# Kernel tuning notes

Measured on AMD Instinct MI355X. Metric: run time of the kernel, lower is better.

The kernel has to match this reference:

```python
import jax, jax.numpy as jnp
import numpy as np
from jax import lax

T, B, F, H = 128, 256, 512, 1024
NEG_SLOPE = 0.01  # torch LeakyReLU default


def leaky_relu(x):
    return jnp.where(x >= 0, x, NEG_SLOPE * x)


def setup_inputs() -> dict:
    key = jax.random.key(0)
    ks = jax.random.split(key, 10)
    s1 = 1.0 / np.sqrt(F)
    sh = 1.0 / np.sqrt(H)
    return {
        "x": jax.random.normal(ks[0], (T, B, F), dtype=jnp.float32),
        "dones": jax.random.randint(ks[1], (T, B), 0, 2, dtype=jnp.int32),
        "W1": jax.random.uniform(ks[2], (H, F), jnp.float32, -s1, s1),
        "b1": jax.random.uniform(ks[3], (H,), jnp.float32, -s1, s1),
        "W_ih": jax.random.uniform(ks[4], (4 * H, H), jnp.float32, -sh, sh),
        "W_hh": jax.random.uniform(ks[5], (4 * H, H), jnp.float32, -sh, sh),
        "b_ih": jax.random.uniform(ks[6], (4 * H,), jnp.float32, -sh, sh),
        "b_hh": jax.random.uniform(ks[7], (4 * H,), jnp.float32, -sh, sh),
        "Wv": jax.random.uniform(ks[8], (1, H), jnp.float32, -sh, sh),
        "bv": jax.random.uniform(ks[9], (1,), jnp.float32, -sh, sh),
    }


def _forward(x, dones, W1, b1, W_ih, W_hh, b_ih, b_hh, Wv, bv):
    # shared_net: Linear + LeakyReLU, applied to all timesteps at once
    shared = leaky_relu(jnp.einsum("tbf,hf->tbh", x, W1) + b1)  # [T,B,H]
    # precompute input contribution to all gates (i,f,g,o order as in torch)
    x_gates = jnp.einsum("tbh,gh->tbg", shared, W_ih) + b_ih + b_hh  # [T,B,4H]
    reset = (dones == 0).astype(x.dtype)[:, :, None]  # [T,B,1], 0 where done

    def step(carry, inp):
        h, c = carry  # [B,H] each
        xg, m = inp
        # mask-reset hidden state where episode ended, then detach (torch .detach())
        h = lax.stop_gradient(h * m)
        c = lax.stop_gradient(c * m)
        gates = xg + h @ W_hh.T  # [B,4H]
        i, f, g, o = jnp.split(gates, 4, axis=-1)
        i = jax.nn.sigmoid(i)
        f = jax.nn.sigmoid(f)
        g = jnp.tanh(g)
        o = jax.nn.sigmoid(o)
        c = f * c + i * g
        h = o * jnp.tanh(c)
        return (h, c), h

    h0 = jnp.zeros((x.shape[1], W_hh.shape[1]), x.dtype)
    (hT, cT), hs = lax.scan(step, (h0, h0), (x_gates, reset))
    value = leaky_relu(hs) @ Wv.T + bv  # [T,B,1]
    hidden = jnp.stack([hT, cT], axis=0)  # [2*num_layers, B, H]
    return value, hidden


def reference(x, dones, W1, b1, W_ih, W_hh, b_ih, b_hh, Wv, bv):
    return _forward(x, dones, W1, b1, W_ih, W_hh, b_ih, b_hh, Wv, bv)
```

## Files before the change

### kernel.cpp

```cpp
#include <hip/hip_runtime.h>
#include <cstdint>
#include <cstddef>

#define T_DIM 128
#define B_DIM 256
#define F_DIM 512
#define H_DIM 1024
#define G_DIM 4096

typedef unsigned short u16;
typedef unsigned short u16x8 __attribute__((ext_vector_type(8)));
typedef unsigned short u16x4 __attribute__((ext_vector_type(4)));
typedef __bf16 bf16x8 __attribute__((ext_vector_type(8)));
typedef float f32x4 __attribute__((ext_vector_type(4)));

__device__ __forceinline__ float bf2f(u16 u) {
    union { unsigned v; float f; } x; x.v = ((unsigned)u) << 16; return x.f;
}
__device__ __forceinline__ u16 f2bf(float f) {
    union { float f; unsigned v; } x; x.f = f;
    return (u16)((x.v + 0x7fffu + ((x.v >> 16) & 1u)) >> 16);
}

__device__ __forceinline__ f32x4 mfma16(u16x8 a, u16x8 b, f32x4 c) {
    return __builtin_amdgcn_mfma_f32_16x16x32_bf16(
        __builtin_bit_cast(bf16x8, a), __builtin_bit_cast(bf16x8, b), c, 0, 0, 0);
}

template <int AUX>
__device__ __forceinline__ void gl_lds16(const void* g, void* s) {
    __builtin_amdgcn_global_load_lds(
        (const __attribute__((address_space(1))) void*)g,
        (__attribute__((address_space(3))) void*)s, 16, 0, AUX);
}

__device__ __forceinline__ float sigm(float x) { return 1.0f / (1.0f + __expf(-x)); }
__device__ __forceinline__ float tanh_fast(float x) {
    float e = __expf(2.0f * x);
    return 1.0f - 2.0f / (e + 1.0f);
}

template <int EPI>
__global__ __launch_bounds__(256) void gemm_bt128(
    const u16* __restrict__ A, const u16* __restrict__ B,
    const float* __restrict__ bias, u16* __restrict__ C, int K, int N) {
    __shared__ __align__(16) u16 smem[128 * 136];
    u16* lA = smem;
    u16* lB = smem + 8192;
    const int lane = threadIdx.x & 63;
    const int wave = threadIdx.x >> 6;
    const int wr = wave >> 1, wc = wave & 1;
    const int bm = blockIdx.x, bn = blockIdx.y;
    f32x4 acc[4][4] = {};
    const int srow = lane >> 3;
    const int scol = (lane & 7) * 8;
    const u16* Abase = A + (size_t)(bm * 128 + srow) * K + scol;
    const u16* Bbase = B + (size_t)(bn * 128 + srow) * K + scol;

    for (int k0 = 0; k0 < K; k0 += 64) {
#pragma unroll
        for (int j = 0; j < 4; ++j) {
            int chunk = wave * 4 + j;
            gl_lds16<0>(Abase + (size_t)(chunk * 8) * K + k0, lA + chunk * 512);
            gl_lds16<0>(Bbase + (size_t)(chunk * 8) * K + k0, lB + chunk * 512);
        }
        __syncthreads();
        const u16* pA = lA + (wr * 64 + (lane & 15)) * 64 + (lane >> 4) * 8;
        const u16* pB = lB + (wc * 64 + (lane & 15)) * 64 + (lane >> 4) * 8;
#pragma unroll
        for (int kk = 0; kk < 2; ++kk) {
            u16x8 a[4], b[4];
#pragma unroll
            for (int m = 0; m < 4; ++m) a[m] = *(const u16x8*)(pA + m * 1024 + kk * 32);
#pragma unroll
            for (int n = 0; n < 4; ++n) b[n] = *(const u16x8*)(pB + n * 1024 + kk * 32);
#pragma unroll
            for (int m = 0; m < 4; ++m)
#pragma unroll
                for (int n = 0; n < 4; ++n)
                    acc[m][n] = mfma16(a[m], b[n], acc[m][n]);
        }
        __syncthreads();
    }
#pragma unroll
    for (int n = 0; n < 4; ++n) {
        int cc = wc * 64 + n * 16 + (lane & 15);
        float bv = bias[bn * 128 + cc];
#pragma unroll
        for (int m = 0; m < 4; ++m) {
            int rr = wr * 64 + m * 16 + ((lane >> 4) * 4);
#pragma unroll
            for (int i = 0; i < 4; ++i) {
                float v = acc[m][n][i] + bv;
                if (EPI == 1) v = (v >= 0.0f) ? v : 0.01f * v;
                smem[(rr + i) * 136 + cc] = f2bf(v);
            }
        }
    }
    __syncthreads();
#pragma unroll
    for (int p = 0; p < 8; ++p) {
        int rr = p * 16 + wave * 4 + (lane >> 4);
        int cc = (lane & 15) * 8;
        u16x8 v = *(const u16x8*)(smem + rr * 136 + cc);
        *(u16x8*)(C + (size_t)(bm * 128 + rr) * N + bn * 128 + cc) = v;
    }
}


template <int AUX>
__device__ __forceinline__ void stage_chunk(const char* panel, char* buf, int kc,
                                            int wave, int lane) {
#pragma unroll
    for (int j = 0; j < 8; ++j) {
        int hr = wave * 8 + j;
        int r = hr * 2 + (lane >> 5);
        int sc = ((lane & 31) * 16) ^ ((r & 7) << 4);
        gl_lds16<AUX>(panel + (size_t)r * 2048 + kc * 512 + sc, buf + (size_t)hr * 1024);
    }
}

__global__ __launch_bounds__(256, 1) void lstm_seq(
    const u16* __restrict__ xg, const u16* __restrict__ Whh,
    const int* __restrict__ dones, const float* __restrict__ Wv,
    u16* __restrict__ h0, u16* __restrict__ h1,
    float* __restrict__ cbuf, float* __restrict__ hbuf,
    float* __restrict__ value, int* __restrict__ flags,
    float* __restrict__ vpartial, int t0, int nt, int first) {
    __shared__ __align__(16) char sm[65536];
    float* lepi = (float*)sm;
    const int tid = threadIdx.x;
    const int lane = tid & 63, wave = tid >> 6;
    const int bm = blockIdx.x & 3, bn = blockIdx.x >> 2;
    const int sw = (lane & 7) << 4;

    u16x8 breg[32];
    {
        const char* wp = (const char*)(Whh + (size_t)(bn * 64) * H_DIM);
        const int rlb = wave * 16 + (lane & 15);
#pragma unroll
        for (int kc = 0; kc < 4; ++kc) {
            char* buf = sm + (kc & 1) * 32768;
            stage_chunk<0>(wp, buf, kc, wave, lane);
            __syncthreads();
#pragma unroll
            for (int s2 = 0; s2 < 8; ++s2) {
                int kb2 = s2 * 64 + (lane >> 4) * 16;
                breg[kc * 8 + s2] = *(const u16x8*)(buf + rlb * 512 + (kb2 ^ sw));
            }
            __syncthreads();
        }
    }

    const int r = tid & 63;
    const int ublk = tid >> 6;
    const int bg = bm * 64 + r;
    const int ucol = bn * 16 + ublk * 4;
    float wv[4], c[4];
#pragma unroll
    for (int uu = 0; uu < 4; ++uu) wv[uu] = Wv[ucol + uu];
    if (first) {
        c[0] = c[1] = c[2] = c[3] = 0.0f;
    } else {
        float4 cv = *(const float4*)(cbuf + (size_t)bg * H_DIM + ucol);
        c[0] = cv.x; c[1] = cv.y; c[2] = cv.z; c[3] = cv.w;
    }

    for (int tt = 0; tt < nt; ++tt) {
        const int t = t0 + tt;
        const u16* hin = (t & 1) ? h1 : h0;
        u16* hout = (t & 1) ? h0 : h1;
        const char* hp = (const char*)(hin + (size_t)(bm * 64) * H_DIM);

        const int done = dones[t * B_DIM + bg];
        u16x4 xv[4];
#pragma unroll
        for (int uu = 0; uu < 4; ++uu)
            xv[uu] = *(const u16x4*)(xg + (size_t)tt * B_DIM * G_DIM +
                                     (size_t)bg * G_DIM + bn * 64 + (ublk * 4 + uu) * 4);

        if (t > 0 && tid < 64) {
            while (__hip_atomic_load(&flags[bm * 64 + tid], __ATOMIC_RELAXED,
                                     __HIP_MEMORY_SCOPE_AGENT) < t)
                __builtin_amdgcn_s_sleep(1);
        }
        __syncthreads();

        stage_chunk<17>(hp, sm, 0, wave, lane);
        if (t > 0 && tid < 64) {
            const float* vp = vpartial + (size_t)((t - 1) & 1) * 65536 +
                              (size_t)(bm * 64 + bn) * 256 + lane * 4;
            union { unsigned long long u; float f[2]; } ua, ub;
            ua.u = __hip_atomic_load((const unsigned long long*)vp, __ATOMIC_RELAXED,
                                     __HIP_MEMORY_SCOPE_AGENT);
            ub.u = __hip_atomic_load((const unsigned long long*)(vp + 2), __ATOMIC_RELAXED,
                                     __HIP_MEMORY_SCOPE_AGENT);
            float s = ua.f[0] + ua.f[1] + ub.f[0] + ub.f[1];
#pragma unroll
            for (int m2 = 32; m2 >= 1; m2 >>= 1) s += __shfl_xor(s, m2);
            if (tid == 0) value[(t - 1) * B_DIM + bm * 64 + bn] += s;
        }
        __syncthreads();

        f32x4 acc[4] = {};
#pragma unroll
        for (int kc = 0; kc < 4; ++kc) {
            char* buf = sm + (kc & 1) * 32768;
            if (kc < 3) stage_chunk<17>(hp, sm + ((kc + 1) & 1) * 32768, kc + 1, wave, lane);
#pragma unroll
            for (int s2 = 0; s2 < 8; ++s2) {
                int kb2 = s2 * 64 + (lane >> 4) * 16;
#pragma unroll
                for (int m = 0; m < 4; ++m) {
                    u16x8 a = *(const u16x8*)(buf + (m * 16 + (lane & 15)) * 512 + (kb2 ^ sw));
                    acc[m] = mfma16(a, breg[kc * 8 + s2], acc[m]);
                }
            }
            __syncthreads();
        }

#pragma unroll
        for (int m = 0; m < 4; ++m)
#pragma unroll
            for (int i = 0; i < 4; ++i)
                lepi[(m * 16 + (lane >> 4) * 4 + i) * 65 + wave * 16 + (lane & 15)] = acc[m][i];
        __syncthreads();

        const float mb = (done == 0) ? 1.0f : 0.0f;
        float vpart = 0.0f;
        u16x4 hb;
        float hf[4];
#pragma unroll
        for (int uu = 0; uu < 4; ++uu) {
            const float* gp = &lepi[r * 65 + (ublk * 4 + uu) * 4];
            float gi = bf2f(xv[uu][0]) + mb * gp[0];
            float gf = bf2f(xv[uu][1]) + mb * gp[1];
            float gg = bf2f(xv[uu][2]) + mb * gp[2];
            float go = bf2f(xv[uu][3]) + mb * gp[3];
            float i_ = sigm(gi), f_ = sigm(gf), g_ = tanh_fast(gg), o_ = sigm(go);
            float cn = f_ * (mb * c[uu]) + i_ * g_;
            float hn = o_ * tanh_fast(cn);
            c[uu] = cn; hf[uu] = hn;
            hb[uu] = f2bf(hn);
            float lr = (hn >= 0.0f) ? hn : 0.01f * hn;
            vpart += lr * wv[uu];
        }
        __hip_atomic_store((unsigned long long*)(hout + (size_t)bg * H_DIM + ucol),
                           __builtin_bit_cast(unsigned long long, hb),
                           __ATOMIC_RELAXED, __HIP_MEMORY_SCOPE_AGENT);
        if (t == T_DIM - 1)
            *(float4*)(hbuf + (size_t)bg * H_DIM + ucol) = make_float4(hf[0], hf[1], hf[2], hf[3]);
        __hip_atomic_store(&vpartial[(size_t)(t & 1) * 65536 + (size_t)bg * 256 + bn * 4 + ublk],
                           vpart, __ATOMIC_RELAXED, __HIP_MEMORY_SCOPE_AGENT);

        __syncthreads();
        if (tid == 0)
            __hip_atomic_store(&flags[bm * 64 + bn], t + 1, __ATOMIC_RELAXED,
                               __HIP_MEMORY_SCOPE_AGENT);
    }
    *(float4*)(cbuf + (size_t)bg * H_DIM + ucol) = make_float4(c[0], c[1], c[2], c[3]);

    if (t0 + nt == T_DIM && tid < 64) {
        while (__hip_atomic_load(&flags[bm * 64 + tid], __ATOMIC_RELAXED,
                                 __HIP_MEMORY_SCOPE_AGENT) < T_DIM)
            __builtin_amdgcn_s_sleep(1);
        const float* vp = vpartial + (size_t)((T_DIM - 1) & 1) * 65536 +
                          (size_t)(bm * 64 + bn) * 256 + lane * 4;
        union { unsigned long long u; float f[2]; } ua, ub;
        ua.u = __hip_atomic_load((const unsigned long long*)vp, __ATOMIC_RELAXED,
                                 __HIP_MEMORY_SCOPE_AGENT);
        ub.u = __hip_atomic_load((const unsigned long long*)(vp + 2), __ATOMIC_RELAXED,
                                 __HIP_MEMORY_SCOPE_AGENT);
        float s = ua.f[0] + ua.f[1] + ub.f[0] + ub.f[1];
#pragma unroll
        for (int m2 = 32; m2 >= 1; m2 >>= 1) s += __shfl_xor(s, m2);
        if (tid == 0) value[(T_DIM - 1) * B_DIM + bm * 64 + bn] += s;
    }
}

__global__ void k_cast_bf16(const float* __restrict__ in, u16* __restrict__ out, int n4) {
    int i = blockIdx.x * 256 + threadIdx.x;
    if (i < n4) {
        float4 v = *(const float4*)(in + (size_t)i * 4);
        u16x4 o;
        o[0] = f2bf(v.x); o[1] = f2bf(v.y); o[2] = f2bf(v.z); o[3] = f2bf(v.w);
        *(u16x4*)(out + (size_t)i * 4) = o;
    }
}

__global__ void k_permute_w(const float* __restrict__ W, u16* __restrict__ Wp) {
    int row = blockIdx.x;
    int rin = (row & 3) * H_DIM + (row >> 2);
    int c = threadIdx.x * 4;
    float4 v = *(const float4*)(W + (size_t)rin * H_DIM + c);
    u16x4 o;
    o[0] = f2bf(v.x); o[1] = f2bf(v.y); o[2] = f2bf(v.z); o[3] = f2bf(v.w);
    *(u16x4*)(Wp + (size_t)row * H_DIM + c) = o;
}

__global__ void k_prep_bias(const float* __restrict__ b_ih, const float* __restrict__ b_hh,
                            float* __restrict__ bc) {
    int i = blockIdx.x * 256 + threadIdx.x;
    int n = i >> 2, q = i & 3;
    bc[i] = b_ih[q * H_DIM + n] + b_hh[q * H_DIM + n];
}

__global__ void k_init(float* __restrict__ value, const float* __restrict__ bv,
                       u16* __restrict__ h0, int* __restrict__ flags) {
    int i = blockIdx.x * 256 + threadIdx.x;
    if (i < B_DIM * H_DIM) h0[i] = 0;
    if (i < T_DIM * B_DIM) value[i] = *bv;
    if (i < 256) flags[i] = 0;
}

extern "C" void kernel_launch(void* const* d_in, const int* in_sizes, int n_in,
                              void* d_out, int out_size, void* d_ws, size_t ws_size,
                              hipStream_t stream) {
    const float* x     = (const float*)d_in[0];
    const int*   dones = (const int*)d_in[1];
    const float* W1    = (const float*)d_in[2];
    const float* b1    = (const float*)d_in[3];
    const float* W_ih  = (const float*)d_in[4];
    const float* W_hh  = (const float*)d_in[5];
    const float* b_ih  = (const float*)d_in[6];
    const float* b_hh  = (const float*)d_in[7];
    const float* Wv    = (const float*)d_in[8];
    const float* bv    = (const float*)d_in[9];

    float* out   = (float*)d_out;
    float* value = out;
    float* hbuf  = out + (size_t)T_DIM * B_DIM;
    float* cbuf  = hbuf + (size_t)B_DIM * H_DIM;

    const size_t per_nt = (size_t)(F_DIM + H_DIM + G_DIM) * B_DIM * 2;
    const size_t fixed = (size_t)H_DIM * F_DIM * 2 + 2 * (size_t)G_DIM * H_DIM * 2 +
                         G_DIM * 4 + 2 * (size_t)B_DIM * H_DIM * 2 +
                         2 * 65536 * 4 + 8192;
    int nt = 2;
    for (int cand = 16; cand >= 2; cand >>= 1)
        if (fixed + (size_t)cand * per_nt + 65536 <= ws_size) { nt = cand; break; }

    char* ws = (char*)d_ws;
    size_t off = 0;
    auto alloc = [&](size_t bytes) {
        void* p = ws + off;
        off = (off + bytes + 255) & ~(size_t)255;
        return p;
    };
    u16*   x_bf   = (u16*)alloc((size_t)nt * B_DIM * F_DIM * 2);
    u16*   shr    = (u16*)alloc((size_t)nt * B_DIM * H_DIM * 2);
    u16*   xg     = (u16*)alloc((size_t)nt * B_DIM * G_DIM * 2);
    u16*   W1b    = (u16*)alloc((size_t)H_DIM * F_DIM * 2);
    u16*   Wihp   = (u16*)alloc((size_t)G_DIM * H_DIM * 2);
    u16*   Whhp   = (u16*)alloc((size_t)G_DIM * H_DIM * 2);
    float* bcomb  = (float*)alloc((size_t)G_DIM * 4);
    u16*   hping  = (u16*)alloc((size_t)B_DIM * H_DIM * 2);
    u16*   hpong  = (u16*)alloc((size_t)B_DIM * H_DIM * 2);
    int*   flags  = (int*)alloc(256 * 4);
    float* vpart  = (float*)alloc(2 * 65536 * 4);

    k_cast_bf16<<<(H_DIM * F_DIM / 4) / 256, 256, 0, stream>>>(W1, W1b, H_DIM * F_DIM / 4);
    k_permute_w<<<G_DIM, 256, 0, stream>>>(W_ih, Wihp);
    k_permute_w<<<G_DIM, 256, 0, stream>>>(W_hh, Whhp);
    k_prep_bias<<<G_DIM / 256, 256, 0, stream>>>(b_ih, b_hh, bcomb);
    k_init<<<(B_DIM * H_DIM) / 256, 256, 0, stream>>>(value, bv, hping, flags);

    for (int t0 = 0; t0 < T_DIM; t0 += nt) {
        int m = nt * B_DIM;
        int n4 = m * F_DIM / 4;
        k_cast_bf16<<<n4 / 256, 256, 0, stream>>>(x + (size_t)t0 * B_DIM * F_DIM, x_bf, n4);
        gemm_bt128<1><<<dim3(m / 128, H_DIM / 128), 256, 0, stream>>>(
            x_bf, W1b, b1, shr, F_DIM, H_DIM);
        gemm_bt128<0><<<dim3(m / 128, G_DIM / 128), 256, 0, stream>>>(
            shr, Wihp, bcomb, xg, H_DIM, G_DIM);

        lstm_seq<<<256, 256, 0, stream>>>(
            xg, Whhp, dones, Wv, hping, hpong, cbuf, hbuf, value, flags, vpart,
            t0, nt, (t0 == 0) ? 1 : 0);
    }
}
```

Before: 1.727 ms.

## Widen LSTM recurrence blocks to 512 threads and enlarge timestep chunks

The persistent recurrent kernel now runs 128 blocks of 512 threads. Each block owns 128 gate columns (32 hidden units) and holds twice the W_hh slice in registers, loaded straight from global memory instead of through LDS. Each timestep now spins on 32 peer flags instead of 64, and the value reduction is spread across two waves. The host also allows up to 64 timesteps per chunk, so fewer GEMM and kernel launches are issued. The cost is fewer CUs used in the latency-bound recurrence and more per-block work, and the final barrier sequence is now executed by only some waves, which may be fragile.

```diff
diff --git a/kernel.cpp b/kernel.cpp
--- a/kernel.cpp
+++ b/kernel.cpp
@@ -109,18 +109,20 @@
 
 
 template <int AUX>
-__device__ __forceinline__ void stage_chunk(const char* panel, char* buf, int kc,
-                                            int wave, int lane) {
-#pragma unroll
-    for (int j = 0; j < 8; ++j) {
-        int hr = wave * 8 + j;
+__device__ __forceinline__ void stage_chunk8(const char* panel, char* buf, int kc,
+                                             int wave, int lane) {
+#pragma unroll
+    for (int j = 0; j < 4; ++j) {
+        int hr = wave * 4 + j;
         int r = hr * 2 + (lane >> 5);
         int sc = ((lane & 31) * 16) ^ ((r & 7) << 4);
         gl_lds16<AUX>(panel + (size_t)r * 2048 + kc * 512 + sc, buf + (size_t)hr * 1024);
     }
 }
 
-__global__ __launch_bounds__(256, 1) void lstm_seq(
+#define LEPI_STRIDE 132
+
+__global__ __launch_bounds__(512, 1) void lstm_seq(
     const u16* __restrict__ xg, const u16* __restrict__ Whh,
     const int* __restrict__ dones, const float* __restrict__ Wv,
     u16* __restrict__ h0, u16* __restrict__ h1,
@@ -136,26 +138,17 @@
 
     u16x8 breg[32];
     {
-        const char* wp = (const char*)(Whh + (size_t)(bn * 64) * H_DIM);
-        const int rlb = wave * 16 + (lane & 15);
-#pragma unroll
-        for (int kc = 0; kc < 4; ++kc) {
-            char* buf = sm + (kc & 1) * 32768;
-            stage_chunk<0>(wp, buf, kc, wave, lane);
-            __syncthreads();
-#pragma unroll
-            for (int s2 = 0; s2 < 8; ++s2) {
-                int kb2 = s2 * 64 + (lane >> 4) * 16;
-                breg[kc * 8 + s2] = *(const u16x8*)(buf + rlb * 512 + (kb2 ^ sw));
-            }
-            __syncthreads();
-        }
+        const u16* wrow = Whh + (size_t)(bn * 128 + wave * 16 + (lane & 15)) * H_DIM +
+                          (lane >> 4) * 8;
+#pragma unroll
+        for (int s = 0; s < 32; ++s)
+            breg[s] = *(const u16x8*)(wrow + s * 32);
     }
 
     const int r = tid & 63;
     const int ublk = tid >> 6;
     const int bg = bm * 64 + r;
-    const int ucol = bn * 16 + ublk * 4;
+    const int ucol = bn * 32 + ublk * 4;
     float wv[4], c[4];
 #pragma unroll
     for (int uu = 0; uu < 4; ++uu) wv[uu] = Wv[ucol + uu];
@@ -177,19 +170,20 @@
 #pragma unroll
         for (int uu = 0; uu < 4; ++uu)
             xv[uu] = *(const u16x4*)(xg + (size_t)tt * B_DIM * G_DIM +
-                                     (size_t)bg * G_DIM + bn * 64 + (ublk * 4 + uu) * 4);
-
-        if (t > 0 && tid < 64) {
-            while (__hip_atomic_load(&flags[bm * 64 + tid], __ATOMIC_RELAXED,
+                                     (size_t)bg * G_DIM + bn * 128 + (ublk * 4 + uu) * 4);
+
+        if (t > 0 && tid < 32) {
+            while (__hip_atomic_load(&flags[bm * 32 + tid], __ATOMIC_RELAXED,
                                      __HIP_MEMORY_SCOPE_AGENT) < t)
                 __builtin_amdgcn_s_sleep(1);
         }
         __syncthreads();
 
-        stage_chunk<17>(hp, sm, 0, wave, lane);
-        if (t > 0 && tid < 64) {
+        stage_chunk8<17>(hp, sm, 0, wave, lane);
+        if (t > 0 && tid < 128) {
+            const int grow = bm * 64 + bn * 2 + (tid >> 6);
             const float* vp = vpartial + (size_t)((t - 1) & 1) * 65536 +
-                              (size_t)(bm * 64 + bn) * 256 + lane * 4;
+                              (size_t)grow * 256 + (tid & 63) * 4;
             union { unsigned long long u; float f[2]; } ua, ub;
             ua.u = __hip_atomic_load((const unsigned long long*)vp, __ATOMIC_RELAXED,
                                      __HIP_MEMORY_SCOPE_AGENT);
@@ -198,7 +192,7 @@
             float s = ua.f[0] + ua.f[1] + ub.f[0] + ub.f[1];
 #pragma unroll
             for (int m2 = 32; m2 >= 1; m2 >>= 1) s += __shfl_xor(s, m2);
-            if (tid == 0) value[(t - 1) * B_DIM + bm * 64 + bn] += s;
+            if ((tid & 63) == 0) value[(t - 1) * B_DIM + grow] += s;
         }
         __syncthreads();
 
@@ -206,7 +200,7 @@
 #pragma unroll
         for (int kc = 0; kc < 4; ++kc) {
             char* buf = sm + (kc & 1) * 32768;
-            if (kc < 3) stage_chunk<17>(hp, sm + ((kc + 1) & 1) * 32768, kc + 1, wave, lane);
+            if (kc < 3) stage_chunk8<17>(hp, sm + ((kc + 1) & 1) * 32768, kc + 1, wave, lane);
 #pragma unroll
             for (int s2 = 0; s2 < 8; ++s2) {
                 int kb2 = s2 * 64 + (lane >> 4) * 16;
@@ -223,7 +217,8 @@
         for (int m = 0; m < 4; ++m)
 #pragma unroll
             for (int i = 0; i < 4; ++i)
-                lepi[(m * 16 + (lane >> 4) * 4 + i) * 65 + wave * 16 + (lane & 15)] = acc[m][i];
+                lepi[(m * 16 + (lane >> 4) * 4 + i) * LEPI_STRIDE + wave * 16 + (lane & 15)] =
+                    acc[m][i];
         __syncthreads();
 
         const float mb = (done == 0) ? 1.0f : 0.0f;
@@ -232,7 +227,7 @@
         float hf[4];
 #pragma unroll
         for (int uu = 0; uu < 4; ++uu) {
-            const float* gp = &lepi[r * 65 + (ublk * 4 + uu) * 4];
+            const float* gp = &lepi[r * LEPI_STRIDE + (ublk * 4 + uu) * 4];
             float gi = bf2f(xv[uu][0]) + mb * gp[0];
             float gf = bf2f(xv[uu][1]) + mb * gp[1];
             float gg = bf2f(xv[uu][2]) + mb * gp[2];
@@ -250,31 +245,40 @@
                            __ATOMIC_RELAXED, __HIP_MEMORY_SCOPE_AGENT);
         if (t == T_DIM - 1)
             *(float4*)(hbuf + (size_t)bg * H_DIM + ucol) = make_float4(hf[0], hf[1], hf[2], hf[3]);
-        __hip_atomic_store(&vpartial[(size_t)(t & 1) * 65536 + (size_t)bg * 256 + bn * 4 + ublk],
+        __hip_atomic_store(&vpartial[(size_t)(t & 1) * 65536 + (size_t)bg * 256 + bn * 8 + ublk],
                            vpart, __ATOMIC_RELAXED, __HIP_MEMORY_SCOPE_AGENT);
 
         __syncthreads();
         if (tid == 0)
-            __hip_atomic_store(&flags[bm * 64 + bn], t + 1, __ATOMIC_RELAXED,
+            __hip_atomic_store(&flags[bm * 32 + bn], t + 1, __ATOMIC_RELAXED,
                                __HIP_MEMORY_SCOPE_AGENT);
     }
     *(float4*)(cbuf + (size_t)bg * H_DIM + ucol) = make_float4(c[0], c[1], c[2], c[3]);
 
-    if (t0 + nt == T_DIM && tid < 64) {
-        while (__hip_atomic_load(&flags[bm * 64 + tid], __ATOMIC_RELAXED,
-                                 __HIP_MEMORY_SCOPE_AGENT) < T_DIM)
-            __builtin_amdgcn_s_sleep(1);
-        const float* vp = vpartial + (size_t)((T_DIM - 1) & 1) * 65536 +
-                          (size_t)(bm * 64 + bn) * 256 + lane * 4;
-        union { unsigned long long u; float f[2]; } ua, ub;
-        ua.u = __hip_atomic_load((const unsigned long long*)vp, __ATOMIC_RELAXED,
-                                 __HIP_MEMORY_SCOPE_AGENT);
-        ub.u = __hip_atomic_load((const unsigned long long*)(vp + 2), __ATOMIC_RELAXED,
-                                 __HIP_MEMORY_SCOPE_AGENT);
-        float s = ua.f[0] + ua.f[1] + ub.f[0] + ub.f[1];
-#pragma unroll
-        for (int m2 = 32; m2 >= 1; m2 >>= 1) s += __shfl_xor(s, m2);
-        if (tid == 0) value[(T_DIM - 1) * B_DIM + bm * 64 + bn] += s;
+    if (t0 + nt == T_DIM && tid < 128) {
+        if (tid < 32) {
+            while (__hip_atomic_load(&flags[bm * 32 + tid], __ATOMIC_RELAXED,
+                                     __HIP_MEMORY_SCOPE_AGENT) < T_DIM)
+                __builtin_amdgcn_s_sleep(1);
+        }
+        __builtin_amdgcn_s_barrier();
+    }
+    if (t0 + nt == T_DIM) {
+        __syncthreads();
+        if (tid < 128) {
+            const int grow = bm * 64 + bn * 2 + (tid >> 6);
+            const float* vp = vpartial + (size_t)((T_DIM - 1) & 1) * 65536 +
+                              (size_t)grow * 256 + (tid & 63) * 4;
+            union { unsigned long long u; float f[2]; } ua, ub;
+            ua.u = __hip_atomic_load((const unsigned long long*)vp, __ATOMIC_RELAXED,
+                                     __HIP_MEMORY_SCOPE_AGENT);
+            ub.u = __hip_atomic_load((const unsigned long long*)(vp + 2), __ATOMIC_RELAXED,
+                                     __HIP_MEMORY_SCOPE_AGENT);
+            float s = ua.f[0] + ua.f[1] + ub.f[0] + ub.f[1];
+#pragma unroll
+            for (int m2 = 32; m2 >= 1; m2 >>= 1) s += __shfl_xor(s, m2);
+            if ((tid & 63) == 0) value[(T_DIM - 1) * B_DIM + grow] += s;
+        }
     }
 }
 
@@ -337,8 +341,9 @@
                          G_DIM * 4 + 2 * (size_t)B_DIM * H_DIM * 2 +
                          2 * 65536 * 4 + 8192;
     int nt = 2;
-    for (int cand = 16; cand >= 2; cand >>= 1)
+    for (int cand = 64; cand >= 2; cand >>= 1)
         if (fixed + (size_t)cand * per_nt + 65536 <= ws_size) { nt = cand; break; }
+    if (nt > T_DIM) nt = T_DIM;
 
     char* ws = (char*)d_ws;
     size_t off = 0;
@@ -374,7 +379,7 @@
         gemm_bt128<0><<<dim3(m / 128, G_DIM / 128), 256, 0, stream>>>(
             shr, Wihp, bcomb, xg, H_DIM, G_DIM);
 
-        lstm_seq<<<256, 256, 0, stream>>>(
+        lstm_seq<<<128, 512, 0, stream>>>(
             xg, Whhp, dones, Wv, hping, hpong, cbuf, hbuf, value, flags, vpart,
             t0, nt, (t0 == 0) ? 1 : 0);
     }
```

New measurement: 1.747 ms. Within noise of the previous version (+1.2%).

## Retile hidden-state layout, stage full h panel in 128KB LDS, coalesce stores

Applied to the files above, without the earlier changes.

Changes the global layout of the ping-pong hidden-state buffer and the value partials to a tiled form. Each block now writes its h tile and value partials with contiguous, coalesced atomic stores after staging them through LDS. When 128KB of dynamic shared memory is available, the whole 64x1024 h panel is loaded in one pass with a single barrier instead of four double-buffered chunks. W_hh fragments are also loaded straight into registers, and the time-chunk size can grow to 64, which cuts the number of launches. The extra LDS round-trip and barrier in the epilogue add some latency to every step.

```diff
diff --git a/kernel.cpp b/kernel.cpp
--- a/kernel.cpp
+++ b/kernel.cpp
@@ -13,6 +13,7 @@
 typedef unsigned short u16x4 __attribute__((ext_vector_type(4)));
 typedef __bf16 bf16x8 __attribute__((ext_vector_type(8)));
 typedef float f32x4 __attribute__((ext_vector_type(4)));
+typedef unsigned long long u64;
 
 __device__ __forceinline__ float bf2f(u16 u) {
     union { unsigned v; float f; } x; x.v = ((unsigned)u) << 16; return x.f;
@@ -107,19 +108,7 @@
     }
 }
 
-
-template <int AUX>
-__device__ __forceinline__ void stage_chunk(const char* panel, char* buf, int kc,
-                                            int wave, int lane) {
-#pragma unroll
-    for (int j = 0; j < 8; ++j) {
-        int hr = wave * 8 + j;
-        int r = hr * 2 + (lane >> 5);
-        int sc = ((lane & 31) * 16) ^ ((r & 7) << 4);
-        gl_lds16<AUX>(panel + (size_t)r * 2048 + kc * 512 + sc, buf + (size_t)hr * 1024);
-    }
-}
-
+template <int FULL>
 __global__ __launch_bounds__(256, 1) void lstm_seq(
     const u16* __restrict__ xg, const u16* __restrict__ Whh,
     const int* __restrict__ dones, const float* __restrict__ Wv,
@@ -127,29 +116,20 @@
     float* __restrict__ cbuf, float* __restrict__ hbuf,
     float* __restrict__ value, int* __restrict__ flags,
     float* __restrict__ vpartial, int t0, int nt, int first) {
-    __shared__ __align__(16) char sm[65536];
+    extern __shared__ __align__(16) char sm[];
     float* lepi = (float*)sm;
+    char* hbB = sm + 20480;
+    float* vpB = (float*)(sm + 24576);
     const int tid = threadIdx.x;
     const int lane = tid & 63, wave = tid >> 6;
     const int bm = blockIdx.x & 3, bn = blockIdx.x >> 2;
-    const int sw = (lane & 7) << 4;
 
     u16x8 breg[32];
     {
-        const char* wp = (const char*)(Whh + (size_t)(bn * 64) * H_DIM);
-        const int rlb = wave * 16 + (lane & 15);
-#pragma unroll
-        for (int kc = 0; kc < 4; ++kc) {
-            char* buf = sm + (kc & 1) * 32768;
-            stage_chunk<0>(wp, buf, kc, wave, lane);
-            __syncthreads();
-#pragma unroll
-            for (int s2 = 0; s2 < 8; ++s2) {
-                int kb2 = s2 * 64 + (lane >> 4) * 16;
-                breg[kc * 8 + s2] = *(const u16x8*)(buf + rlb * 512 + (kb2 ^ sw));
-            }
-            __syncthreads();
-        }
+        const u16* wrow = Whh + (size_t)(bn * 64 + wave * 16 + (lane & 15)) * H_DIM +
+                          (lane >> 4) * 8;
+#pragma unroll
+        for (int s = 0; s < 32; ++s) breg[s] = *(const u16x8*)(wrow + s * 32);
     }
 
     const int r = tid & 63;
@@ -166,11 +146,13 @@
         c[0] = cv.x; c[1] = cv.y; c[2] = cv.z; c[3] = cv.w;
     }
 
+    const int rl = lane & 15;
+    const int ko = (lane >> 4) * 16;
+
     for (int tt = 0; tt < nt; ++tt) {
         const int t = t0 + tt;
-        const u16* hin = (t & 1) ? h1 : h0;
-        u16* hout = (t & 1) ? h0 : h1;
-        const char* hp = (const char*)(hin + (size_t)(bm * 64) * H_DIM);
+        const char* hinB = (const char*)((t & 1) ? h1 : h0);
+        u16* houtB = (t & 1) ? h0 : h1;
 
         const int done = dones[t * B_DIM + bg];
         u16x4 xv[4];
@@ -186,38 +168,85 @@
         }
         __syncthreads();
 
-        stage_chunk<17>(hp, sm, 0, wave, lane);
-        if (t > 0 && tid < 64) {
-            const float* vp = vpartial + (size_t)((t - 1) & 1) * 65536 +
-                              (size_t)(bm * 64 + bn) * 256 + lane * 4;
-            union { unsigned long long u; float f[2]; } ua, ub;
-            ua.u = __hip_atomic_load((const unsigned long long*)vp, __ATOMIC_RELAXED,
-                                     __HIP_MEMORY_SCOPE_AGENT);
-            ub.u = __hip_atomic_load((const unsigned long long*)(vp + 2), __ATOMIC_RELAXED,
-                                     __HIP_MEMORY_SCOPE_AGENT);
-            float s = ua.f[0] + ua.f[1] + ub.f[0] + ub.f[1];
-#pragma unroll
-            for (int m2 = 32; m2 >= 1; m2 >>= 1) s += __shfl_xor(s, m2);
-            if (tid == 0) value[(t - 1) * B_DIM + bm * 64 + bn] += s;
-        }
-        __syncthreads();
-
         f32x4 acc[4] = {};
-#pragma unroll
-        for (int kc = 0; kc < 4; ++kc) {
-            char* buf = sm + (kc & 1) * 32768;
-            if (kc < 3) stage_chunk<17>(hp, sm + ((kc + 1) & 1) * 32768, kc + 1, wave, lane);
-#pragma unroll
-            for (int s2 = 0; s2 < 8; ++s2) {
-                int kb2 = s2 * 64 + (lane >> 4) * 16;
+        if (FULL) {
+#pragma unroll
+            for (int l = 0; l < 32; ++l) {
+                int o = l * 4096 + wave * 1024 + lane * 16;
+                int row = o >> 11;
+                int cg = (o & 2047) ^ ((row & 7) << 4);
+                gl_lds16<17>(hinB + (size_t)(cg >> 5) * 8192 + bm * 2048 + row * 32 + (cg & 31),
+                             sm + o);
+            }
+            if (t > 0 && tid < 64) {
+                const float* vp = vpartial + (size_t)((t - 1) & 1) * 65536 +
+                                  (size_t)lane * 1024 + (size_t)(bm * 64 + bn) * 4;
+                union { u64 u; float f[2]; } ua, ub;
+                ua.u = __hip_atomic_load((const u64*)vp, __ATOMIC_RELAXED,
+                                         __HIP_MEMORY_SCOPE_AGENT);
+                ub.u = __hip_atomic_load((const u64*)(vp + 2), __ATOMIC_RELAXED,
+                                         __HIP_MEMORY_SCOPE_AGENT);
+                float s = ua.f[0] + ua.f[1] + ub.f[0] + ub.f[1];
+#pragma unroll
+                for (int m2 = 32; m2 >= 1; m2 >>= 1) s += __shfl_xor(s, m2);
+                if (tid == 0) value[(t - 1) * B_DIM + bm * 64 + bn] += s;
+            }
+            __syncthreads();
+
+#pragma unroll
+            for (int s = 0; s < 32; ++s) {
 #pragma unroll
                 for (int m = 0; m < 4; ++m) {
-                    u16x8 a = *(const u16x8*)(buf + (m * 16 + (lane & 15)) * 512 + (kb2 ^ sw));
-                    acc[m] = mfma16(a, breg[kc * 8 + s2], acc[m]);
+                    int row = m * 16 + rl;
+                    u16x8 a = *(const u16x8*)(sm + row * 2048 +
+                                              ((s * 64 + ko) ^ ((row & 7) << 4)));
+                    acc[m] = mfma16(a, breg[s], acc[m]);
                 }
             }
+        } else {
+            auto stage = [&](int kc, char* buf) {
+#pragma unroll
+                for (int l = 0; l < 8; ++l) {
+                    int o = l * 4096 + wave * 1024 + lane * 16;
+                    int row = o >> 9;
+                    int cg = (kc << 9) + ((o & 511) ^ ((row & 7) << 4));
+                    gl_lds16<17>(hinB + (size_t)(cg >> 5) * 8192 + bm * 2048 + row * 32 +
+                                 (cg & 31), buf + o);
+                }
+            };
+            stage(0, sm);
+            if (t > 0 && tid < 64) {
+                const float* vp = vpartial + (size_t)((t - 1) & 1) * 65536 +
+                                  (size_t)lane * 1024 + (size_t)(bm * 64 + bn) * 4;
+                union { u64 u; float f[2]; } ua, ub;
+                ua.u = __hip_atomic_load((const u64*)vp, __ATOMIC_RELAXED,
+                                         __HIP_MEMORY_SCOPE_AGENT);
+                ub.u = __hip_atomic_load((const u64*)(vp + 2), __ATOMIC_RELAXED,
+                                         __HIP_MEMORY_SCOPE_AGENT);
+                float s = ua.f[0] + ua.f[1] + ub.f[0] + ub.f[1];
+#pragma unroll
+                for (int m2 = 32; m2 >= 1; m2 >>= 1) s += __shfl_xor(s, m2);
+                if (tid == 0) value[(t - 1) * B_DIM + bm * 64 + bn] += s;
+            }
             __syncthreads();
-        }
+#pragma unroll
+            for (int kc = 0; kc < 4; ++kc) {
+                char* buf = sm + (kc & 1) * 32768;
+                if (kc < 3) stage(kc + 1, sm + ((kc + 1) & 1) * 32768);
+#pragma unroll
+                for (int s2 = 0; s2 < 8; ++s2) {
+#pragma unroll
+                    for (int m = 0; m < 4; ++m) {
+                        int row = m * 16 + rl;
+                        u16x8 a = *(const u16x8*)(buf + row * 512 +
+                                                  ((s2 * 64 + ko) ^ ((row & 7) << 4)));
+                        acc[m] = mfma16(a, breg[kc * 8 + s2], acc[m]);
+                    }
+                }
+                __syncthreads();
+            }
+        }
+        __syncthreads();
 
 #pragma unroll
         for (int m = 0; m < 4; ++m)
@@ -245,14 +274,25 @@
             float lr = (hn >= 0.0f) ? hn : 0.01f * hn;
             vpart += lr * wv[uu];
         }
-        __hip_atomic_store((unsigned long long*)(hout + (size_t)bg * H_DIM + ucol),
-                           __builtin_bit_cast(unsigned long long, hb),
-                           __ATOMIC_RELAXED, __HIP_MEMORY_SCOPE_AGENT);
+        *(u16x4*)(hbB + r * 32 + ublk * 8) = hb;
+        vpB[r * 4 + ublk] = vpart;
         if (t == T_DIM - 1)
             *(float4*)(hbuf + (size_t)bg * H_DIM + ucol) = make_float4(hf[0], hf[1], hf[2], hf[3]);
-        __hip_atomic_store(&vpartial[(size_t)(t & 1) * 65536 + (size_t)bg * 256 + bn * 4 + ublk],
-                           vpart, __ATOMIC_RELAXED, __HIP_MEMORY_SCOPE_AGENT);
-
+        __syncthreads();
+
+        {
+            u64 hv = *(const u64*)(hbB + tid * 8);
+            __hip_atomic_store((u64*)((char*)houtB + (size_t)bn * 8192 + bm * 2048 + tid * 8),
+                               hv, __ATOMIC_RELAXED, __HIP_MEMORY_SCOPE_AGENT);
+            if (tid < 64) {
+                const u64* pv = (const u64*)vpB + tid * 2;
+                u64 v0 = pv[0], v1 = pv[1];
+                float* dv = vpartial + (size_t)(t & 1) * 65536 + (size_t)bn * 1024 +
+                            bm * 256 + tid * 4;
+                __hip_atomic_store((u64*)dv, v0, __ATOMIC_RELAXED, __HIP_MEMORY_SCOPE_AGENT);
+                __hip_atomic_store((u64*)dv + 1, v1, __ATOMIC_RELAXED, __HIP_MEMORY_SCOPE_AGENT);
+            }
+        }
         __syncthreads();
         if (tid == 0)
             __hip_atomic_store(&flags[bm * 64 + bn], t + 1, __ATOMIC_RELAXED,
@@ -265,11 +305,10 @@
                                  __HIP_MEMORY_SCOPE_AGENT) < T_DIM)
             __builtin_amdgcn_s_sleep(1);
         const float* vp = vpartial + (size_t)((T_DIM - 1) & 1) * 65536 +
-                          (size_t)(bm * 64 + bn) * 256 + lane * 4;
-        union { unsigned long long u; float f[2]; } ua, ub;
-        ua.u = __hip_atomic_load((const unsigned long long*)vp, __ATOMIC_RELAXED,
-                                 __HIP_MEMORY_SCOPE_AGENT);
-        ub.u = __hip_atomic_load((const unsigned long long*)(vp + 2), __ATOMIC_RELAXED,
+                          (size_t)lane * 1024 + (size_t)(bm * 64 + bn) * 4;
+        union { u64 u; float f[2]; } ua, ub;
+        ua.u = __hip_atomic_load((const u64*)vp, __ATOMIC_RELAXED, __HIP_MEMORY_SCOPE_AGENT);
+        ub.u = __hip_atomic_load((const u64*)(vp + 2), __ATOMIC_RELAXED,
                                  __HIP_MEMORY_SCOPE_AGENT);
         float s = ua.f[0] + ua.f[1] + ub.f[0] + ub.f[1];
 #pragma unroll
@@ -337,8 +376,9 @@
                          G_DIM * 4 + 2 * (size_t)B_DIM * H_DIM * 2 +
                          2 * 65536 * 4 + 8192;
     int nt = 2;
-    for (int cand = 16; cand >= 2; cand >>= 1)
+    for (int cand = 64; cand >= 2; cand >>= 1)
         if (fixed + (size_t)cand * per_nt + 65536 <= ws_size) { nt = cand; break; }
+    if (nt > T_DIM) nt = T_DIM;
 
     char* ws = (char*)d_ws;
     size_t off = 0;
@@ -359,6 +399,10 @@
     int*   flags  = (int*)alloc(256 * 4);
     float* vpart  = (float*)alloc(2 * 65536 * 4);
 
+    int full = (hipFuncSetAttribute(reinterpret_cast<const void*>(&lstm_seq<1>),
+                                    hipFuncAttributeMaxDynamicSharedMemorySize,
+                                    131072) == hipSuccess) ? 1 : 0;
+
     k_cast_bf16<<<(H_DIM * F_DIM / 4) / 256, 256, 0, stream>>>(W1, W1b, H_DIM * F_DIM / 4);
     k_permute_w<<<G_DIM, 256, 0, stream>>>(W_ih, Wihp);
     k_permute_w<<<G_DIM, 256, 0, stream>>>(W_hh, Whhp);
@@ -374,8 +418,13 @@
         gemm_bt128<0><<<dim3(m / 128, G_DIM / 128), 256, 0, stream>>>(
             shr, Wihp, bcomb, xg, H_DIM, G_DIM);
 
-        lstm_seq<<<256, 256, 0, stream>>>(
-            xg, Whhp, dones, Wv, hping, hpong, cbuf, hbuf, value, flags, vpart,
-            t0, nt, (t0 == 0) ? 1 : 0);
-    }
-}
+        if (full)
+            lstm_seq<1><<<256, 256, 131072, stream>>>(
+                xg, Whhp, dones, Wv, hping, hpong, cbuf, hbuf, value, flags, vpart,
+                t0, nt, (t0 == 0) ? 1 : 0);
+        else
+            lstm_seq<0><<<256, 256, 65536, stream>>>(
+                xg, Whhp, dones, Wv, hping, hpong, cbuf, hbuf, value, flags, vpart,
+                t0, nt, (t0 == 0) ? 1 : 0);
+    }
+}
```

Result: slower. 1.982 ms (+14.8%).

## Block-tile hidden state layout, stage outputs through LDS, trim LSTM step barriers

Applied to the files above, without the earlier changes.

Changes the global layout of the ping-pong hidden-state buffers and value partials to a per-block tiled layout. Each block now stages its h tile and value partials in LDS and writes them out as contiguous coalesced stores, so consumers read contiguous chunks. Every wave now polls the flags directly, which removes a barrier, and two further barriers per step are dropped. W_hh registers are also loaded straight from global memory instead of through LDS. The aim is to cut per-timestep synchronisation and scattered store latency on the sequential critical path, at the cost of more flag-polling traffic and an extra LDS round trip.

```diff
diff --git a/kernel.cpp b/kernel.cpp
--- a/kernel.cpp
+++ b/kernel.cpp
@@ -13,6 +13,7 @@
 typedef unsigned short u16x4 __attribute__((ext_vector_type(4)));
 typedef __bf16 bf16x8 __attribute__((ext_vector_type(8)));
 typedef float f32x4 __attribute__((ext_vector_type(4)));
+typedef unsigned long long u64;
 
 __device__ __forceinline__ float bf2f(u16 u) {
     union { unsigned v; float f; } x; x.v = ((unsigned)u) << 16; return x.f;
@@ -108,15 +109,16 @@
 }
 
 
-template <int AUX>
-__device__ __forceinline__ void stage_chunk(const char* panel, char* buf, int kc,
-                                            int wave, int lane) {
+__device__ __forceinline__ void stage_chunk_blk(const char* hinB, int bm, char* buf,
+                                                int kc, int wave, int lane) {
 #pragma unroll
     for (int j = 0; j < 8; ++j) {
         int hr = wave * 8 + j;
         int r = hr * 2 + (lane >> 5);
         int sc = ((lane & 31) * 16) ^ ((r & 7) << 4);
-        gl_lds16<AUX>(panel + (size_t)r * 2048 + kc * 512 + sc, buf + (size_t)hr * 1024);
+        int cbg = kc * 512 + sc;
+        gl_lds16<17>(hinB + (size_t)(cbg >> 5) * 8192 + bm * 2048 + r * 32 + (cbg & 31),
+                     buf + (size_t)hr * 1024);
     }
 }
 
@@ -129,6 +131,8 @@
     float* __restrict__ vpartial, int t0, int nt, int first) {
     __shared__ __align__(16) char sm[65536];
     float* lepi = (float*)sm;
+    char* hbB = sm + 17408;
+    float* vpB = (float*)(sm + 19456);
     const int tid = threadIdx.x;
     const int lane = tid & 63, wave = tid >> 6;
     const int bm = blockIdx.x & 3, bn = blockIdx.x >> 2;
@@ -136,20 +140,10 @@
 
     u16x8 breg[32];
     {
-        const char* wp = (const char*)(Whh + (size_t)(bn * 64) * H_DIM);
-        const int rlb = wave * 16 + (lane & 15);
-#pragma unroll
-        for (int kc = 0; kc < 4; ++kc) {
-            char* buf = sm + (kc & 1) * 32768;
-            stage_chunk<0>(wp, buf, kc, wave, lane);
-            __syncthreads();
-#pragma unroll
-            for (int s2 = 0; s2 < 8; ++s2) {
-                int kb2 = s2 * 64 + (lane >> 4) * 16;
-                breg[kc * 8 + s2] = *(const u16x8*)(buf + rlb * 512 + (kb2 ^ sw));
-            }
-            __syncthreads();
-        }
+        const u16* wrow = Whh + (size_t)(bn * 64 + wave * 16 + (lane & 15)) * H_DIM +
+                          (lane >> 4) * 8;
+#pragma unroll
+        for (int s = 0; s < 32; ++s) breg[s] = *(const u16x8*)(wrow + s * 32);
     }
 
     const int r = tid & 63;
@@ -166,11 +160,13 @@
         c[0] = cv.x; c[1] = cv.y; c[2] = cv.z; c[3] = cv.w;
     }
 
+    const int rl = lane & 15;
+    const int ko = (lane >> 4) * 16;
+
     for (int tt = 0; tt < nt; ++tt) {
         const int t = t0 + tt;
-        const u16* hin = (t & 1) ? h1 : h0;
-        u16* hout = (t & 1) ? h0 : h1;
-        const char* hp = (const char*)(hin + (size_t)(bm * 64) * H_DIM);
+        const char* hinB = (const char*)((t & 1) ? h1 : h0);
+        u16* houtB = (t & 1) ? h0 : h1;
 
         const int done = dones[t * B_DIM + bg];
         u16x4 xv[4];
@@ -179,21 +175,20 @@
             xv[uu] = *(const u16x4*)(xg + (size_t)tt * B_DIM * G_DIM +
                                      (size_t)bg * G_DIM + bn * 64 + (ublk * 4 + uu) * 4);
 
-        if (t > 0 && tid < 64) {
-            while (__hip_atomic_load(&flags[bm * 64 + tid], __ATOMIC_RELAXED,
+        if (t > 0) {
+            while (__hip_atomic_load(&flags[bm * 64 + lane], __ATOMIC_RELAXED,
                                      __HIP_MEMORY_SCOPE_AGENT) < t)
                 __builtin_amdgcn_s_sleep(1);
         }
-        __syncthreads();
-
-        stage_chunk<17>(hp, sm, 0, wave, lane);
+
+        stage_chunk_blk(hinB, bm, sm, 0, wave, lane);
         if (t > 0 && tid < 64) {
             const float* vp = vpartial + (size_t)((t - 1) & 1) * 65536 +
-                              (size_t)(bm * 64 + bn) * 256 + lane * 4;
-            union { unsigned long long u; float f[2]; } ua, ub;
-            ua.u = __hip_atomic_load((const unsigned long long*)vp, __ATOMIC_RELAXED,
+                              (size_t)lane * 1024 + (size_t)(bm * 64 + bn) * 4;
+            union { u64 u; float f[2]; } ua, ub;
+            ua.u = __hip_atomic_load((const u64*)vp, __ATOMIC_RELAXED,
                                      __HIP_MEMORY_SCOPE_AGENT);
-            ub.u = __hip_atomic_load((const unsigned long long*)(vp + 2), __ATOMIC_RELAXED,
+            ub.u = __hip_atomic_load((const u64*)(vp + 2), __ATOMIC_RELAXED,
                                      __HIP_MEMORY_SCOPE_AGENT);
             float s = ua.f[0] + ua.f[1] + ub.f[0] + ub.f[1];
 #pragma unroll
@@ -206,25 +201,25 @@
 #pragma unroll
         for (int kc = 0; kc < 4; ++kc) {
             char* buf = sm + (kc & 1) * 32768;
-            if (kc < 3) stage_chunk<17>(hp, sm + ((kc + 1) & 1) * 32768, kc + 1, wave, lane);
+            if (kc < 3) stage_chunk_blk(hinB, bm, sm + ((kc + 1) & 1) * 32768, kc + 1,
+                                        wave, lane);
 #pragma unroll
             for (int s2 = 0; s2 < 8; ++s2) {
-                int kb2 = s2 * 64 + (lane >> 4) * 16;
+                int kb2 = s2 * 64 + ko;
 #pragma unroll
                 for (int m = 0; m < 4; ++m) {
-                    u16x8 a = *(const u16x8*)(buf + (m * 16 + (lane & 15)) * 512 + (kb2 ^ sw));
+                    u16x8 a = *(const u16x8*)(buf + (m * 16 + rl) * 512 + (kb2 ^ sw));
                     acc[m] = mfma16(a, breg[kc * 8 + s2], acc[m]);
                 }
             }
-            __syncthreads();
+            if (kc < 3) __syncthreads();
         }
 
 #pragma unroll
         for (int m = 0; m < 4; ++m)
 #pragma unroll
             for (int i = 0; i < 4; ++i)
-                lepi[(m * 16 + (lane >> 4) * 4 + i) * 65 + wave * 16 + (lane & 15)] = acc[m][i];
-        __syncthreads();
+                lepi[(m * 16 + (lane >> 4) * 4 + i) * 65 + wave * 16 + rl] = acc[m][i];
 
         const float mb = (done == 0) ? 1.0f : 0.0f;
         float vpart = 0.0f;
@@ -245,14 +240,25 @@
             float lr = (hn >= 0.0f) ? hn : 0.01f * hn;
             vpart += lr * wv[uu];
         }
-        __hip_atomic_store((unsigned long long*)(hout + (size_t)bg * H_DIM + ucol),
-                           __builtin_bit_cast(unsigned long long, hb),
-                           __ATOMIC_RELAXED, __HIP_MEMORY_SCOPE_AGENT);
+        *(u16x4*)(hbB + r * 32 + ublk * 8) = hb;
+        vpB[r * 4 + ublk] = vpart;
         if (t == T_DIM - 1)
             *(float4*)(hbuf + (size_t)bg * H_DIM + ucol) = make_float4(hf[0], hf[1], hf[2], hf[3]);
-        __hip_atomic_store(&vpartial[(size_t)(t & 1) * 65536 + (size_t)bg * 256 + bn * 4 + ublk],
-                           vpart, __ATOMIC_RELAXED, __HIP_MEMORY_SCOPE_AGENT);
-
+        __syncthreads();
+
+        {
+            u64 hv = *(const u64*)(hbB + tid * 8);
+            __hip_atomic_store((u64*)((char*)houtB + (size_t)bn * 8192 + bm * 2048 + tid * 8),
+                               hv, __ATOMIC_RELAXED, __HIP_MEMORY_SCOPE_AGENT);
+            if (tid < 64) {
+                const u64* pv = (const u64*)vpB + tid * 2;
+                u64 v0 = pv[0], v1 = pv[1];
+                float* dv = vpartial + (size_t)(t & 1) * 65536 + (size_t)bn * 1024 +
+                            bm * 256 + tid * 4;
+                __hip_atomic_store((u64*)dv, v0, __ATOMIC_RELAXED, __HIP_MEMORY_SCOPE_AGENT);
+                __hip_atomic_store((u64*)dv + 1, v1, __ATOMIC_RELAXED, __HIP_MEMORY_SCOPE_AGENT);
+            }
+        }
         __syncthreads();
         if (tid == 0)
             __hip_atomic_store(&flags[bm * 64 + bn], t + 1, __ATOMIC_RELAXED,
@@ -261,15 +267,14 @@
     *(float4*)(cbuf + (size_t)bg * H_DIM + ucol) = make_float4(c[0], c[1], c[2], c[3]);
 
     if (t0 + nt == T_DIM && tid < 64) {
-        while (__hip_atomic_load(&flags[bm * 64 + tid], __ATOMIC_RELAXED,
+        while (__hip_atomic_load(&flags[bm * 64 + lane], __ATOMIC_RELAXED,
                                  __HIP_MEMORY_SCOPE_AGENT) < T_DIM)
             __builtin_amdgcn_s_sleep(1);
         const float* vp = vpartial + (size_t)((T_DIM - 1) & 1) * 65536 +
-                          (size_t)(bm * 64 + bn) * 256 + lane * 4;
-        union { unsigned long long u; float f[2]; } ua, ub;
-        ua.u = __hip_atomic_load((const unsigned long long*)vp, __ATOMIC_RELAXED,
-                                 __HIP_MEMORY_SCOPE_AGENT);
-        ub.u = __hip_atomic_load((const unsigned long long*)(vp + 2), __ATOMIC_RELAXED,
+                          (size_t)lane * 1024 + (size_t)(bm * 64 + bn) * 4;
+        union { u64 u; float f[2]; } ua, ub;
+        ua.u = __hip_atomic_load((const u64*)vp, __ATOMIC_RELAXED, __HIP_MEMORY_SCOPE_AGENT);
+        ub.u = __hip_atomic_load((const u64*)(vp + 2), __ATOMIC_RELAXED,
                                  __HIP_MEMORY_SCOPE_AGENT);
         float s = ua.f[0] + ua.f[1] + ub.f[0] + ub.f[1];
 #pragma unroll
```

After: 1.613 ms. -6.6%, faster.
